# Optimization experiments

Measured on AMD Instinct MI355X. Metric: run time of the kernel, lower is better.

## Reference

```python
import jax, jax.numpy as jnp
import numpy as np

FACTOR = 5

def setup_inputs() -> dict:
    key = jax.random.key(0)
    k1, k2, k3, k4 = jax.random.split(key, 4)
    B, L, E = 64, 4096, 64
    sample_k = min(FACTOR * int(np.ceil(np.log(L))), L)  # 45
    return {
        "queries": jax.random.normal(k1, (B, L, E), dtype=jnp.float32),
        "keys": jax.random.normal(k2, (B, L, E), dtype=jnp.float32),
        "values": jax.random.normal(k3, (B, L, E), dtype=jnp.float32),
        "index_sample": jax.random.randint(k4, (L, sample_k), 0, L, dtype=jnp.int32),
    }

def reference(queries, keys, values, index_sample):
    B, L_Q, D = queries.shape
    _, L_K, _ = keys.shape
    u = min(FACTOR * int(np.ceil(np.log(L_Q))), L_Q)  # n_top queries

    # --- _prob_QK: random K-sample gather + sparsity measure + topk ---
    # K_sample: (B, L_Q, sample_k, E) via gather (no dense K_expand materialized)
    K_sample = keys[:, index_sample, :]
    Q_K_sample = jnp.einsum('ble,blse->bls', queries, K_sample)
    M = Q_K_sample.max(-1) - Q_K_sample.sum(-1) / L_K  # (B, L_Q)
    _, M_top = jax.lax.top_k(M, u)  # (B, u) indices of top queries

    Q_reduce = jnp.take_along_axis(queries, M_top[:, :, None], axis=1)  # (B, u, E)
    scores_top = jnp.einsum('bue,bke->buk', Q_reduce, keys)  # (B, u, L_K)

    scale = 1.0 / np.sqrt(D)
    scores_top = scores_top * scale

    # --- _get_initial_context: mask_flag=True -> cumulative sum of V ---
    context = jnp.cumsum(values, axis=-2)  # (B, L_Q, D)

    # --- _update_context: softmax over full keys, scatter into context rows ---
    attn = jax.nn.softmax(scores_top, axis=-1)  # (B, u, L_K)
    upd = jnp.einsum('buk,bkd->bud', attn, values)  # (B, u, D)
    context = context.at[jnp.arange(B)[:, None], M_top, :].set(upd)
    return context
```

## Files before the change

kernel.cpp:

```cpp
#include <hip/hip_runtime.h>

#define Bv 64
#define Lv 4096
#define Dv 64
#define Uv 45
#define UP 48
#define NC 32
#define CKK 128
#define NJ 4
#define UPP 52
#define NSUB 64

#define OFF_M    0
#define SZ_M     (Bv*Lv)
#define OFF_QR   (OFF_M + SZ_M)
#define SZ_QR    (Bv*UP*Dv)
#define OFF_PMS  (OFF_QR + SZ_QR)
#define SZ_PMS   (Bv*NC*2*UP)
#define OFF_DEN  (OFF_PMS + SZ_PMS)
#define SZ_DEN   (Bv*2*UP)
#define OFF_UPD  (OFF_DEN + SZ_DEN)
#define SZ_UPD   (Bv*UP*Dv)
#define OFF_CS   (OFF_UPD + SZ_UPD)
#define SZ_CS    (Bv*NSUB*Dv)
#define OFF_TOP  (OFF_CS + SZ_CS)
#define SZ_TOP   (Bv*Uv)

__global__ __launch_bounds__(256) void k_M(const float* __restrict__ Q,
                                           const float* __restrict__ K,
                                           const int* __restrict__ idx,
                                           float* __restrict__ Mout) {
  __shared__ int sidx[32 * Uv];
  int i = blockIdx.x;
  int x = i & 7, j = i >> 3;
  int b = x + 8 * (j >> 7);
  int w = j & 127;
  int t = threadIdx.x;
  for (int p = t; p < 32 * Uv; p += 256) sidx[p] = idx[(w * 32) * Uv + p];
  int g = t >> 3, lane = t & 7;
  int l = w * 32 + g;
  const float4* qr = (const float4*)(Q + ((size_t)b * Lv + l) * Dv + lane * 8);
  float4 q0 = qr[0], q1 = qr[1];
  const char* Kb = (const char*)(K + (size_t)b * Lv * Dv) + lane * 32;
  __syncthreads();
  float mx = -3.0e38f, sm = 0.f;
#pragma unroll 3
  for (int s = 0; s < Uv; s++) {
    int ki = sidx[g * Uv + s];
    const float4* kr = (const float4*)(Kb + (size_t)ki * 256);
    float4 k0 = kr[0], k1 = kr[1];
    float d = q0.x * k0.x + q0.y * k0.y + q0.z * k0.z + q0.w * k0.w
            + q1.x * k1.x + q1.y * k1.y + q1.z * k1.z + q1.w * k1.w;
    d += __shfl_xor(d, 1);
    d += __shfl_xor(d, 2);
    d += __shfl_xor(d, 4);
    mx = fmaxf(mx, d);
    sm += d;
  }
  if (lane == 0) Mout[(size_t)b * Lv + l] = mx - sm * (1.0f / (float)Lv);
}

__global__ __launch_bounds__(1024) void k_topk(const float* __restrict__ M,
                                               const float* __restrict__ Q,
                                               int* __restrict__ Mtop,
                                               float* __restrict__ Qr) {
  __shared__ float wv[16];
  __shared__ int wi[16];
  __shared__ int win_i_s;
  __shared__ int list[Uv];
  int b = blockIdx.x;
  int t = threadIdx.x;
  const float* Mb = M + (size_t)b * Lv;
  float r0 = Mb[t], r1 = Mb[t + 1024], r2 = Mb[t + 2048], r3 = Mb[t + 3072];
  int wave = t >> 6, lane = t & 63;
  for (int it = 0; it < Uv; it++) {
    float bv = r0; int bi = t;
    if (r1 > bv) { bv = r1; bi = t + 1024; }
    if (r2 > bv) { bv = r2; bi = t + 2048; }
    if (r3 > bv) { bv = r3; bi = t + 3072; }
#pragma unroll
    for (int off = 1; off < 64; off <<= 1) {
      float v2 = __shfl_xor(bv, off);
      int i2 = __shfl_xor(bi, off);
      if (v2 > bv || (v2 == bv && i2 < bi)) { bv = v2; bi = i2; }
    }
    if (lane == 0) { wv[wave] = bv; wi[wave] = bi; }
    __syncthreads();
    if (t < 64) {
      float cv = (lane < 16) ? wv[lane] : -3.0e38f;
      int ci = (lane < 16) ? wi[lane] : (1 << 30);
#pragma unroll
      for (int off = 1; off < 16; off <<= 1) {
        float v2 = __shfl_xor(cv, off);
        int i2 = __shfl_xor(ci, off);
        if (v2 > cv || (v2 == cv && i2 < ci)) { cv = v2; ci = i2; }
      }
      if (lane == 0) { win_i_s = ci; list[it] = ci; }
    }
    __syncthreads();
    int wn = win_i_s;
    if ((wn & 1023) == t) {
      int c = wn >> 10;
      if (c == 0) r0 = -3.0e38f;
      else if (c == 1) r1 = -3.0e38f;
      else if (c == 2) r2 = -3.0e38f;
      else r3 = -3.0e38f;
    }
    __syncthreads();
  }
  if (t < Uv) Mtop[b * Uv + t] = list[t];
  for (int p = t; p < UP * Dv; p += 1024) {
    int u = p >> 6, e = p & 63;
    float v = 0.f;
    if (u < Uv) {
      int row = list[u];
      v = Q[((size_t)b * Lv + row) * Dv + e] * 0.125f;
    }
    Qr[((size_t)b * UP + u) * Dv + e] = v;
  }
}

#define STAGE_QST(QS, QR, b)                                        \
  for (int i_ = threadIdx.x; i_ < Dv * UP; i_ += blockDim.x) {      \
    int u_ = i_ >> 6, e_ = i_ & 63;                                 \
    QS[e_ * UPP + u_] = QR[((size_t)(b) * UP + u_) * Dv + e_];      \
  }

#define SCORE_TILE(ACC, QS, KMAT, b_, c_, ug_, kg_)                                   \
  {                                                                                    \
    const float* Kb_ = (KMAT) + ((size_t)(b_) * Lv + (size_t)(c_) * CKK + (kg_)) * Dv; \
    for (int e = 0; e < Dv; e += 4) {                                                  \
      float qq[4][8];                                                                  \
      _Pragma("unroll")                                                                \
      for (int e2 = 0; e2 < 4; e2++) {                                                 \
        float4 qa = *(const float4*)&(QS)[(e + e2) * UPP + (ug_) * 8];                 \
        float4 qb = *(const float4*)&(QS)[(e + e2) * UPP + (ug_) * 8 + 4];             \
        qq[e2][0]=qa.x; qq[e2][1]=qa.y; qq[e2][2]=qa.z; qq[e2][3]=qa.w;                \
        qq[e2][4]=qb.x; qq[e2][5]=qb.y; qq[e2][6]=qb.z; qq[e2][7]=qb.w;                \
      }                                                                                \
      _Pragma("unroll")                                                                \
      for (int j = 0; j < NJ; j++) {                                                   \
        float4 kv = *(const float4*)(Kb_ + (size_t)(32 * j) * Dv + e);                 \
        _Pragma("unroll")                                                              \
        for (int uu = 0; uu < 8; uu++)                                                 \
          ACC[uu][j] += qq[0][uu]*kv.x + qq[1][uu]*kv.y + qq[2][uu]*kv.z + qq[3][uu]*kv.w; \
      }                                                                                \
    }                                                                                  \
  }

__global__ __launch_bounds__(192) void k_ms(const float* __restrict__ Kmat,
                                            const float* __restrict__ Qr,
                                            float* __restrict__ pms) {
  __shared__ float qsT[Dv * UPP];
  int b = blockIdx.x >> 5, c = blockIdx.x & 31;
  STAGE_QST(qsT, Qr, b);
  __syncthreads();
  int t = threadIdx.x, ug = t >> 5, kg = t & 31;
  float acc[8][NJ];
#pragma unroll
  for (int uu = 0; uu < 8; uu++)
#pragma unroll
    for (int j = 0; j < NJ; j++) acc[uu][j] = 0.f;
  SCORE_TILE(acc, qsT, Kmat, b, c, ug, kg);
#pragma unroll
  for (int uu = 0; uu < 8; uu++) {
    float m = acc[uu][0];
#pragma unroll
    for (int j = 1; j < NJ; j++) m = fmaxf(m, acc[uu][j]);
#pragma unroll
    for (int off = 1; off < 32; off <<= 1) m = fmaxf(m, __shfl_xor(m, off));
    float s = 0.f;
#pragma unroll
    for (int j = 0; j < NJ; j++) s += __expf(acc[uu][j] - m);
#pragma unroll
    for (int off = 1; off < 32; off <<= 1) s += __shfl_xor(s, off);
    if (kg == 0) {
      pms[(((size_t)b * NC + c) * 2 + 0) * UP + ug * 8 + uu] = m;
      pms[(((size_t)b * NC + c) * 2 + 1) * UP + ug * 8 + uu] = s;
    }
  }
}

__global__ __launch_bounds__(64) void k_den(const float* __restrict__ pms,
                                            float* __restrict__ den) {
  int b = blockIdx.x, u = threadIdx.x;
  if (u >= UP) return;
  float mx = -3.0e38f;
  for (int c = 0; c < NC; c++)
    mx = fmaxf(mx, pms[(((size_t)b * NC + c) * 2 + 0) * UP + u]);
  float d = 0.f;
  for (int c = 0; c < NC; c++)
    d += pms[(((size_t)b * NC + c) * 2 + 1) * UP + u] *
         __expf(pms[(((size_t)b * NC + c) * 2 + 0) * UP + u] - mx);
  den[(size_t)b * 2 * UP + u] = mx;
  den[(size_t)b * 2 * UP + UP + u] = 1.f / d;
}

__global__ __launch_bounds__(256) void k_zero(float4* __restrict__ upd4) {
  upd4[blockIdx.x * 256 + threadIdx.x] = make_float4(0.f, 0.f, 0.f, 0.f);
}

__global__ __launch_bounds__(192) void k_pv(const float* __restrict__ Kmat,
                                            const float* __restrict__ V,
                                            const float* __restrict__ Qr,
                                            const float* __restrict__ den,
                                            float* __restrict__ upd) {
  __shared__ float qsT[Dv * UPP];
  __shared__ float wl[UP * CKK];
  int b = blockIdx.x >> 5, c = blockIdx.x & 31;
  STAGE_QST(qsT, Qr, b);
  __syncthreads();
  int t = threadIdx.x, ug = t >> 5, kg = t & 31;
  {
    float acc[8][NJ];
#pragma unroll
    for (int uu = 0; uu < 8; uu++)
#pragma unroll
      for (int j = 0; j < NJ; j++) acc[uu][j] = 0.f;
    SCORE_TILE(acc, qsT, Kmat, b, c, ug, kg);
#pragma unroll
    for (int uu = 0; uu < 8; uu++) {
      float mx = den[(size_t)b * 2 * UP + ug * 8 + uu];
      float iv = den[(size_t)b * 2 * UP + UP + ug * 8 + uu];
#pragma unroll
      for (int j = 0; j < NJ; j++)
        wl[(ug * 8 + uu) * CKK + kg + 32 * j] = __expf(acc[uu][j] - mx) * iv;
    }
  }
  __syncthreads();
  int w = t >> 6, lane = t & 63;
  float acc2[16];
#pragma unroll
  for (int uu = 0; uu < 16; uu++) acc2[uu] = 0.f;
  const float* Vb = V + ((size_t)b * Lv + (size_t)c * CKK) * Dv;
  for (int k4 = 0; k4 < CKK; k4 += 4) {
    float v0 = Vb[(size_t)(k4 + 0) * Dv + lane];
    float v1 = Vb[(size_t)(k4 + 1) * Dv + lane];
    float v2 = Vb[(size_t)(k4 + 2) * Dv + lane];
    float v3 = Vb[(size_t)(k4 + 3) * Dv + lane];
#pragma unroll
    for (int uu = 0; uu < 16; uu++) {
      float4 w4 = *(const float4*)&wl[(w * 16 + uu) * CKK + k4];
      acc2[uu] += w4.x * v0 + w4.y * v1 + w4.z * v2 + w4.w * v3;
    }
  }
#pragma unroll
  for (int uu = 0; uu < 16; uu++)
    atomicAdd(&upd[((size_t)b * UP + w * 16 + uu) * Dv + lane], acc2[uu]);
}

__global__ __launch_bounds__(256) void k_cs1(const float* __restrict__ V,
                                             float* __restrict__ cs) {
  int b = blockIdx.x >> 4, c4 = blockIdx.x & 15;
  int g = threadIdx.x >> 6, d = threadIdx.x & 63;
  int sub = c4 * 4 + g;
  const float* Vb = V + ((size_t)b * Lv + sub * 64) * Dv + d;
  float acc = 0.f;
  for (int r = 0; r < 64; r++) acc += Vb[(size_t)r * Dv];
  cs[((size_t)b * NSUB + sub) * Dv + d] = acc;
}

__global__ __launch_bounds__(256) void k_cs3(const float* __restrict__ V,
                                             const float* __restrict__ cs,
                                             float* __restrict__ out) {
  int b = blockIdx.x >> 4, c4 = blockIdx.x & 15;
  int g = threadIdx.x >> 6, d = threadIdx.x & 63;
  int sub = c4 * 4 + g;
  float acc = 0.f;
  for (int s = 0; s < sub; s++) acc += cs[((size_t)b * NSUB + s) * Dv + d];
  const float* Vb = V + ((size_t)b * Lv + sub * 64) * Dv + d;
  float* Ob = out + ((size_t)b * Lv + sub * 64) * Dv + d;
  for (int r = 0; r < 64; r++) {
    acc += Vb[(size_t)r * Dv];
    Ob[(size_t)r * Dv] = acc;
  }
}

__global__ __launch_bounds__(64) void k_upd(const float* __restrict__ upd,
                                            const int* __restrict__ Mtop,
                                            float* __restrict__ out) {
  int b = blockIdx.x / Uv, u = blockIdx.x % Uv;
  int d = threadIdx.x;
  float s = upd[((size_t)b * UP + u) * Dv + d];
  int row = Mtop[b * Uv + u];
  out[((size_t)b * Lv + row) * Dv + d] = s;
}

extern "C" void kernel_launch(void* const* d_in, const int* in_sizes, int n_in,
                              void* d_out, int out_size, void* d_ws, size_t ws_size,
                              hipStream_t stream) {
  (void)in_sizes; (void)n_in; (void)out_size; (void)ws_size;
  const float* Q = (const float*)d_in[0];
  const float* K = (const float*)d_in[1];
  const float* V = (const float*)d_in[2];
  const int* idx = (const int*)d_in[3];
  float* out = (float*)d_out;
  float* wsf = (float*)d_ws;
  float* M   = wsf + OFF_M;
  float* Qr  = wsf + OFF_QR;
  float* pms = wsf + OFF_PMS;
  float* den = wsf + OFF_DEN;
  float* upd = wsf + OFF_UPD;
  float* cs  = wsf + OFF_CS;
  int* top   = (int*)(wsf + OFF_TOP);

  k_M<<<8192, 256, 0, stream>>>(Q, K, idx, M);
  k_topk<<<Bv, 1024, 0, stream>>>(M, Q, top, Qr);
  k_ms<<<Bv * NC, 192, 0, stream>>>(K, Qr, pms);
  k_den<<<Bv, 64, 0, stream>>>(pms, den);
  k_zero<<<(Bv * UP * Dv) / 1024, 256, 0, stream>>>((float4*)upd);
  k_pv<<<Bv * NC, 192, 0, stream>>>(K, V, Qr, den, upd);
  k_cs1<<<1024, 256, 0, stream>>>(V, cs);
  k_cs3<<<1024, 256, 0, stream>>>(V, cs, out);
  k_upd<<<Bv * Uv, 64, 0, stream>>>(upd, top, out);
}
```

Measured before the change: 575.5 us.

## Drop max-pass softmax, accumulate denominators atomically, fuse cumsum partials and zeroing

Removes the separate score/max pass (k_ms) and the denominator kernel (k_den). k_pv now writes unnormalized exp(score) weights and atomically adds per-query row sums to a denominator buffer, and k_upd divides by that sum at the end. This saves a full extra read of K and the score recomputation. The V block partial sums for the cumsum and the zeroing of upd/den are folded into k_M, and the cumsum chunking is changed to 32 rows to match. Skipping max subtraction risks exp overflow if scores are large, and the float atomics make the reduction order nondeterministic.

```diff
diff --git a/kernel.cpp b/kernel.cpp
--- a/kernel.cpp
+++ b/kernel.cpp
@@ -9,33 +9,37 @@
 #define CKK 128
 #define NJ 4
 #define UPP 52
-#define NSUB 64
+#define NSUB 128
 
 #define OFF_M    0
 #define SZ_M     (Bv*Lv)
 #define OFF_QR   (OFF_M + SZ_M)
 #define SZ_QR    (Bv*UP*Dv)
-#define OFF_PMS  (OFF_QR + SZ_QR)
-#define SZ_PMS   (Bv*NC*2*UP)
-#define OFF_DEN  (OFF_PMS + SZ_PMS)
-#define SZ_DEN   (Bv*2*UP)
-#define OFF_UPD  (OFF_DEN + SZ_DEN)
+#define OFF_UPD  (OFF_QR + SZ_QR)
 #define SZ_UPD   (Bv*UP*Dv)
-#define OFF_CS   (OFF_UPD + SZ_UPD)
+#define OFF_DEN  (OFF_UPD + SZ_UPD)
+#define SZ_DEN   (Bv*UP)
+#define OFF_CS   (OFF_DEN + SZ_DEN)
 #define SZ_CS    (Bv*NSUB*Dv)
 #define OFF_TOP  (OFF_CS + SZ_CS)
 #define SZ_TOP   (Bv*Uv)
+#define NZBLK 195
 
 __global__ __launch_bounds__(256) void k_M(const float* __restrict__ Q,
                                            const float* __restrict__ K,
+                                           const float* __restrict__ V,
                                            const int* __restrict__ idx,
-                                           float* __restrict__ Mout) {
+                                           float* __restrict__ Mout,
+                                           float* __restrict__ cs,
+                                           float4* __restrict__ zbuf) {
   __shared__ int sidx[32 * Uv];
+  __shared__ float sp[4][Dv];
   int i = blockIdx.x;
   int x = i & 7, j = i >> 3;
   int b = x + 8 * (j >> 7);
   int w = j & 127;
   int t = threadIdx.x;
+  if (i < NZBLK) zbuf[(i << 8) + t] = make_float4(0.f, 0.f, 0.f, 0.f);
   for (int p = t; p < 32 * Uv; p += 256) sidx[p] = idx[(w * 32) * Uv + p];
   int g = t >> 3, lane = t & 7;
   int l = w * 32 + g;
@@ -58,6 +62,15 @@
     sm += d;
   }
   if (lane == 0) Mout[(size_t)b * Lv + l] = mx - sm * (1.0f / (float)Lv);
+  int d = t & 63, rq = t >> 6;
+  const float* Vb = V + ((size_t)b * Lv + w * 32 + rq * 8) * Dv + d;
+  float a = 0.f;
+#pragma unroll
+  for (int r = 0; r < 8; r++) a += Vb[(size_t)r * Dv];
+  sp[rq][d] = a;
+  __syncthreads();
+  if (t < 64) cs[((size_t)b * NSUB + w) * Dv + t] =
+      sp[0][t] + sp[1][t] + sp[2][t] + sp[3][t];
 }
 
 __global__ __launch_bounds__(1024) void k_topk(const float* __restrict__ M,
@@ -144,67 +157,15 @@
         _Pragma("unroll")                                                              \
         for (int uu = 0; uu < 8; uu++)                                                 \
           ACC[uu][j] += qq[0][uu]*kv.x + qq[1][uu]*kv.y + qq[2][uu]*kv.z + qq[3][uu]*kv.w; \
-      }                                                                                \
+      }                                                                                  \
     }                                                                                  \
   }
-
-__global__ __launch_bounds__(192) void k_ms(const float* __restrict__ Kmat,
-                                            const float* __restrict__ Qr,
-                                            float* __restrict__ pms) {
-  __shared__ float qsT[Dv * UPP];
-  int b = blockIdx.x >> 5, c = blockIdx.x & 31;
-  STAGE_QST(qsT, Qr, b);
-  __syncthreads();
-  int t = threadIdx.x, ug = t >> 5, kg = t & 31;
-  float acc[8][NJ];
-#pragma unroll
-  for (int uu = 0; uu < 8; uu++)
-#pragma unroll
-    for (int j = 0; j < NJ; j++) acc[uu][j] = 0.f;
-  SCORE_TILE(acc, qsT, Kmat, b, c, ug, kg);
-#pragma unroll
-  for (int uu = 0; uu < 8; uu++) {
-    float m = acc[uu][0];
-#pragma unroll
-    for (int j = 1; j < NJ; j++) m = fmaxf(m, acc[uu][j]);
-#pragma unroll
-    for (int off = 1; off < 32; off <<= 1) m = fmaxf(m, __shfl_xor(m, off));
-    float s = 0.f;
-#pragma unroll
-    for (int j = 0; j < NJ; j++) s += __expf(acc[uu][j] - m);
-#pragma unroll
-    for (int off = 1; off < 32; off <<= 1) s += __shfl_xor(s, off);
-    if (kg == 0) {
-      pms[(((size_t)b * NC + c) * 2 + 0) * UP + ug * 8 + uu] = m;
-      pms[(((size_t)b * NC + c) * 2 + 1) * UP + ug * 8 + uu] = s;
-    }
-  }
-}
-
-__global__ __launch_bounds__(64) void k_den(const float* __restrict__ pms,
-                                            float* __restrict__ den) {
-  int b = blockIdx.x, u = threadIdx.x;
-  if (u >= UP) return;
-  float mx = -3.0e38f;
-  for (int c = 0; c < NC; c++)
-    mx = fmaxf(mx, pms[(((size_t)b * NC + c) * 2 + 0) * UP + u]);
-  float d = 0.f;
-  for (int c = 0; c < NC; c++)
-    d += pms[(((size_t)b * NC + c) * 2 + 1) * UP + u] *
-         __expf(pms[(((size_t)b * NC + c) * 2 + 0) * UP + u] - mx);
-  den[(size_t)b * 2 * UP + u] = mx;
-  den[(size_t)b * 2 * UP + UP + u] = 1.f / d;
-}
-
-__global__ __launch_bounds__(256) void k_zero(float4* __restrict__ upd4) {
-  upd4[blockIdx.x * 256 + threadIdx.x] = make_float4(0.f, 0.f, 0.f, 0.f);
-}
 
 __global__ __launch_bounds__(192) void k_pv(const float* __restrict__ Kmat,
                                             const float* __restrict__ V,
                                             const float* __restrict__ Qr,
-                                            const float* __restrict__ den,
-                                            float* __restrict__ upd) {
+                                            float* __restrict__ upd,
+                                            float* __restrict__ den) {
   __shared__ float qsT[Dv * UPP];
   __shared__ float wl[UP * CKK];
   int b = blockIdx.x >> 5, c = blockIdx.x & 31;
@@ -220,11 +181,16 @@
     SCORE_TILE(acc, qsT, Kmat, b, c, ug, kg);
 #pragma unroll
     for (int uu = 0; uu < 8; uu++) {
-      float mx = den[(size_t)b * 2 * UP + ug * 8 + uu];
-      float iv = den[(size_t)b * 2 * UP + UP + ug * 8 + uu];
-#pragma unroll
-      for (int j = 0; j < NJ; j++)
-        wl[(ug * 8 + uu) * CKK + kg + 32 * j] = __expf(acc[uu][j] - mx) * iv;
+      float dsum = 0.f;
+#pragma unroll
+      for (int j = 0; j < NJ; j++) {
+        float wgt = __expf(acc[uu][j]);
+        wl[(ug * 8 + uu) * CKK + kg + 32 * j] = wgt;
+        dsum += wgt;
+      }
+#pragma unroll
+      for (int off = 1; off < 32; off <<= 1) dsum += __shfl_xor(dsum, off);
+      if (kg == 0) atomicAdd(&den[b * UP + ug * 8 + uu], dsum);
     }
   }
   __syncthreads();
@@ -249,39 +215,30 @@
     atomicAdd(&upd[((size_t)b * UP + w * 16 + uu) * Dv + lane], acc2[uu]);
 }
 
-__global__ __launch_bounds__(256) void k_cs1(const float* __restrict__ V,
-                                             float* __restrict__ cs) {
-  int b = blockIdx.x >> 4, c4 = blockIdx.x & 15;
-  int g = threadIdx.x >> 6, d = threadIdx.x & 63;
-  int sub = c4 * 4 + g;
-  const float* Vb = V + ((size_t)b * Lv + sub * 64) * Dv + d;
-  float acc = 0.f;
-  for (int r = 0; r < 64; r++) acc += Vb[(size_t)r * Dv];
-  cs[((size_t)b * NSUB + sub) * Dv + d] = acc;
-}
-
 __global__ __launch_bounds__(256) void k_cs3(const float* __restrict__ V,
                                              const float* __restrict__ cs,
                                              float* __restrict__ out) {
-  int b = blockIdx.x >> 4, c4 = blockIdx.x & 15;
+  int b = blockIdx.x >> 5, c4 = blockIdx.x & 31;
   int g = threadIdx.x >> 6, d = threadIdx.x & 63;
   int sub = c4 * 4 + g;
   float acc = 0.f;
   for (int s = 0; s < sub; s++) acc += cs[((size_t)b * NSUB + s) * Dv + d];
-  const float* Vb = V + ((size_t)b * Lv + sub * 64) * Dv + d;
-  float* Ob = out + ((size_t)b * Lv + sub * 64) * Dv + d;
-  for (int r = 0; r < 64; r++) {
+  const float* Vb = V + ((size_t)b * Lv + sub * 32) * Dv + d;
+  float* Ob = out + ((size_t)b * Lv + sub * 32) * Dv + d;
+  for (int r = 0; r < 32; r++) {
     acc += Vb[(size_t)r * Dv];
     Ob[(size_t)r * Dv] = acc;
   }
 }
 
 __global__ __launch_bounds__(64) void k_upd(const float* __restrict__ upd,
+                                            const float* __restrict__ den,
                                             const int* __restrict__ Mtop,
                                             float* __restrict__ out) {
   int b = blockIdx.x / Uv, u = blockIdx.x % Uv;
   int d = threadIdx.x;
-  float s = upd[((size_t)b * UP + u) * Dv + d];
+  float inv = 1.0f / den[b * UP + u];
+  float s = upd[((size_t)b * UP + u) * Dv + d] * inv;
   int row = Mtop[b * Uv + u];
   out[((size_t)b * Lv + row) * Dv + d] = s;
 }
@@ -298,19 +255,14 @@
   float* wsf = (float*)d_ws;
   float* M   = wsf + OFF_M;
   float* Qr  = wsf + OFF_QR;
-  float* pms = wsf + OFF_PMS;
+  float* upd = wsf + OFF_UPD;
   float* den = wsf + OFF_DEN;
-  float* upd = wsf + OFF_UPD;
   float* cs  = wsf + OFF_CS;
   int* top   = (int*)(wsf + OFF_TOP);
 
-  k_M<<<8192, 256, 0, stream>>>(Q, K, idx, M);
+  k_M<<<8192, 256, 0, stream>>>(Q, K, V, idx, M, cs, (float4*)upd);
   k_topk<<<Bv, 1024, 0, stream>>>(M, Q, top, Qr);
-  k_ms<<<Bv * NC, 192, 0, stream>>>(K, Qr, pms);
-  k_den<<<Bv, 64, 0, stream>>>(pms, den);
-  k_zero<<<(Bv * UP * Dv) / 1024, 256, 0, stream>>>((float4*)upd);
-  k_pv<<<Bv * NC, 192, 0, stream>>>(K, V, Qr, den, upd);
-  k_cs1<<<1024, 256, 0, stream>>>(V, cs);
-  k_cs3<<<1024, 256, 0, stream>>>(V, cs, out);
-  k_upd<<<Bv * Uv, 64, 0, stream>>>(upd, top, out);
-}
+  k_pv<<<Bv * NC, 192, 0, stream>>>(K, V, Qr, upd, den);
+  k_cs3<<<Bv * 32, 256, 0, stream>>>(V, cs, out);
+  k_upd<<<Bv * Uv, 64, 0, stream>>>(upd, den, top, out);
+}
```

Result: faster. 528.4 us (-8.2%).
